# Performance work log

Measured on AMD Instinct MI355X. Metric: run time of the kernel, lower is better.

## Reference

```python
import jax, jax.numpy as jnp
import numpy as np

NUM_HEADS = 16
ROPE_BASE = 10000.0
NEG_INF = -1e9


def _layer_norm(x, g, b, eps=1e-5):
    mu = jnp.mean(x, axis=-1, keepdims=True)
    var = jnp.mean(jnp.square(x - mu), axis=-1, keepdims=True)
    return (x - mu) * jax.lax.rsqrt(var + eps) * g + b


def _rope_tables(seq_len, width):
    # theta_i = base^(-2i/width); tables shape (seq_len, width) with [m*theta, m*theta] concat
    theta = jnp.power(ROPE_BASE, -jnp.arange(0, width, 2, dtype=jnp.float32) / width)
    m_theta = jnp.arange(seq_len, dtype=jnp.float32)[:, None] * theta[None, :]
    m_theta = jnp.concatenate([m_theta, m_theta], axis=-1)
    return jnp.cos(m_theta), jnp.sin(m_theta)


def _apply_rope(x, cos, sin):
    # x: (BH, T, D); cos/sin: (T, D)
    half = x.shape[-1] // 2
    rot = jnp.concatenate([-x[..., half:], x[..., :half]], axis=-1)
    return cos[None] * x + sin[None] * rot


def setup_inputs() -> dict:
    key = jax.random.key(0)
    ks = jax.random.split(key, 6)
    T, B, C, F = 2048, 2, 1024, 4096
    s = 0.02
    return {
        "x": jax.random.normal(ks[0], (T, B, C), jnp.float32),
        "in_w": jax.random.normal(ks[1], (3 * C, C), jnp.float32) * s,
        "in_b": jnp.zeros((3 * C,), jnp.float32),
        "out_w": jax.random.normal(ks[2], (C, C), jnp.float32) * s,
        "out_b": jnp.zeros((C,), jnp.float32),
        "ln1_g": jnp.ones((C,), jnp.float32),
        "ln1_b": jnp.zeros((C,), jnp.float32),
        "ln2_g": jnp.ones((C,), jnp.float32),
        "ln2_b": jnp.zeros((C,), jnp.float32),
        "w1": jax.random.normal(ks[3], (F, C), jnp.float32) * s,
        "b1": jnp.zeros((F,), jnp.float32),
        "w2": jax.random.normal(ks[4], (C, F), jnp.float32) * s,
        "b2": jnp.zeros((C,), jnp.float32),
    }


def reference(x, in_w, in_b, out_w, out_b, ln1_g, ln1_b, ln2_g, ln2_b, w1, b1, w2, b2):
    # x: (T, B, C)  fairseq Time x Batch x Channel
    T, B, C = x.shape
    H = NUM_HEADS
    D = C // H

    # --- self-attention block (pre-LN) ---
    residual = x
    h = _layer_norm(x, ln1_g, ln1_b)
    qkv = h @ in_w.T + in_b                       # (T, B, 3C)
    q, k, v = jnp.split(qkv, 3, axis=-1)
    q = q * (D ** -0.5)

    def to_heads(t):  # (T, B, C) -> (B*H, T, D)
        return t.reshape(T, B * H, D).transpose(1, 0, 2)

    q, k, v = to_heads(q), to_heads(k), to_heads(v)
    cos, sin = _rope_tables(T, D)
    q = _apply_rope(q, cos, sin)
    k = _apply_rope(k, cos, sin)

    scores = jnp.einsum("btd,bsd->bts", q, k)     # (B*H, T, T)
    causal = jnp.triu(jnp.ones((T, T), dtype=bool), k=1)
    scores = jnp.where(causal[None], jnp.float32(NEG_INF), scores)
    attn = jax.nn.softmax(scores, axis=-1)
    o = jnp.einsum("bts,bsd->btd", attn, v)       # (B*H, T, D)
    o = o.transpose(1, 0, 2).reshape(T, B, C)
    o = o @ out_w.T + out_b
    x = residual + o

    # --- FFN block (pre-LN) ---
    residual = x
    h = _layer_norm(x, ln2_g, ln2_b)
    h = jax.nn.gelu(h @ w1.T + b1)
    h = h @ w2.T + b2
    return residual + h
```

## Files before the change

### kernel.cpp

```cpp
#include <hip/hip_runtime.h>
#include <hip/hip_bf16.h>
#include <math.h>

#define T_LEN 2048
#define B_SZ  2
#define C_DIM 1024
#define H_NUM 16
#define D_HEAD 64
#define F_DIM 4096
#define NT    (T_LEN * B_SZ)
#define BH    (B_SZ * H_NUM)
#define C3    (3 * C_DIM)

typedef __attribute__((ext_vector_type(8))) short short8v;
typedef __attribute__((ext_vector_type(4))) float f32x4;
typedef __hip_bfloat16 bf16;

__device__ __forceinline__ float bf2f(bf16 v) { return __bfloat162float(v); }
__device__ __forceinline__ bf16  f2bf(float f) { return __float2bfloat16(f); }
__device__ __forceinline__ short f2bfs(float f) { bf16 h = __float2bfloat16(f); return *(short*)&h; }
__device__ __forceinline__ void split2(float v, short& h, short& l) {
    bf16 hb = __float2bfloat16(v);
    bf16 lb = __float2bfloat16(v - __bfloat162float(hb));
    h = *(short*)&hb; l = *(short*)&lb;
}
__device__ __forceinline__ f32x4 mfma16(short8v a, short8v b, f32x4 c) {
    return __builtin_amdgcn_mfma_f32_16x16x32_bf16(a, b, c, 0, 0, 0);
}
__device__ __forceinline__ void async16(const void* g, void* lds) {
    __builtin_amdgcn_global_load_lds(
        (const __attribute__((address_space(1))) void*)g,
        (__attribute__((address_space(3))) void*)lds, 16, 0, 0);
}

__device__ __forceinline__ float block_sum_256(float val, float* sred) {
#pragma unroll
    for (int off = 32; off > 0; off >>= 1)
        val += __shfl_down(val, off, 64);
    int lane = threadIdx.x & 63;
    int wid  = threadIdx.x >> 6;
    if (lane == 0) sred[wid] = val;
    __syncthreads();
    float r = sred[0] + sred[1] + sred[2] + sred[3];
    __syncthreads();
    return r;
}

__global__ __launch_bounds__(256) void split_kernel(const float* __restrict__ src,
                                                    bf16* __restrict__ hi, bf16* __restrict__ lo) {
    int i = blockIdx.x * 256 + threadIdx.x;
    float4 v = ((const float4*)src)[i];
    short4 hv, lv;
    split2(v.x, hv.x, lv.x); split2(v.y, hv.y, lv.y);
    split2(v.z, hv.z, lv.z); split2(v.w, hv.w, lv.w);
    ((short4*)hi)[i] = hv;
    ((short4*)lo)[i] = lv;
}

__global__ __launch_bounds__(256) void ln_split_kernel(const float* __restrict__ x,
                                                       const float* __restrict__ g,
                                                       const float* __restrict__ b,
                                                       bf16* __restrict__ oh, bf16* __restrict__ ol) {
    __shared__ float sred[4];
    int row = blockIdx.x;
    int tid = threadIdx.x;
    const float* xr = x + (size_t)row * C_DIM;
    float4 xv = *(const float4*)(xr + tid * 4);
    float s = xv.x + xv.y + xv.z + xv.w;
    s = block_sum_256(s, sred);
    float mu = s * (1.0f / C_DIM);
    float d0 = xv.x - mu, d1 = xv.y - mu, d2 = xv.z - mu, d3 = xv.w - mu;
    float vs = d0 * d0 + d1 * d1 + d2 * d2 + d3 * d3;
    vs = block_sum_256(vs, sred);
    float rstd = rsqrtf(vs * (1.0f / C_DIM) + 1e-5f);
    float4 gv = *(const float4*)(g + tid * 4);
    float4 bv = *(const float4*)(b + tid * 4);
    float y0 = d0 * rstd * gv.x + bv.x, y1 = d1 * rstd * gv.y + bv.y;
    float y2 = d2 * rstd * gv.z + bv.z, y3 = d3 * rstd * gv.w + bv.w;
    short4 hv, lv;
    split2(y0, hv.x, lv.x); split2(y1, hv.y, lv.y);
    split2(y2, hv.z, lv.z); split2(y3, hv.w, lv.w);
    size_t base = (size_t)row * C_DIM / 4 + tid;
    ((short4*)oh)[base] = hv;
    ((short4*)ol)[base] = lv;
}

template <int EPI, bool ASPLIT, bool OUTBF16>
__global__ __launch_bounds__(256) void gemm_bf16(const bf16* __restrict__ Ah, const bf16* __restrict__ Al,
                                                 const bf16* __restrict__ Bh, const bf16* __restrict__ Bl,
                                                 const float* __restrict__ bias, const float* __restrict__ res,
                                                 float* __restrict__ Cf, bf16* __restrict__ Cb,
                                                 int N, int K) {
    constexpr int NBUF = ASPLIT ? 4 : 3;
    __shared__ __align__(16) char LDS[2][NBUF * 8192];

    int tid = threadIdx.x;
    int w = tid >> 6, l = tid & 63;
    int c = l & 15, g4 = l >> 4;
    int wm = w >> 1, wn = w & 1;
    int bn = blockIdx.x, bm = blockIdx.y;

    f32x4 acc[4][4];
#pragma unroll
    for (int i = 0; i < 4; i++)
#pragma unroll
        for (int j = 0; j < 4; j++) acc[i][j] = (f32x4){0.f, 0.f, 0.f, 0.f};

    const bf16* gB[4];
    gB[0] = Ah + (size_t)bm * 128 * K;
    gB[1] = Bh + (size_t)bn * 128 * K;
    gB[2] = Bl + (size_t)bn * 128 * K;
    gB[3] = ASPLIT ? (Al + (size_t)bm * 128 * K) : gB[0];
    const int NSEG = NBUF * 8;
    int lr4 = l >> 2, lc4 = l & 3;

    auto STAGE = [&](int kt, int pg) {
#pragma unroll
        for (int sidx = w; sidx < NSEG; sidx += 4) {
            int bsel = sidx >> 3, seg = sidx & 7;
            int r = seg * 16 + lr4;
            int cs = lc4 ^ ((r >> 1) & 3);
            const bf16* g = gB[bsel] + (size_t)r * K + kt + cs * 8;
            async16(g, LDS[pg] + bsel * 8192 + seg * 1024);
        }
    };

    STAGE(0, 0);
    __syncthreads();
    int cur = 0;
    for (int kt = 0; kt < K; kt += 32) {
        if (kt + 32 < K) STAGE(kt + 32, cur ^ 1);

        char* base = LDS[cur];
        char* LAhB = base;
        char* LBhB = base + 8192;
        char* LBlB = base + 16384;
        char* LAlB = base + 24576;

        short8v fah[4], fal[4], fbh[4], fbl[4];
#pragma unroll
        for (int i = 0; i < 4; i++) {
            int row = wm * 64 + i * 16 + c;
            int off = row * 64 + 16 * (g4 ^ ((row >> 1) & 3));
            fah[i] = *(const short8v*)(LAhB + off);
            if (ASPLIT) fal[i] = *(const short8v*)(LAlB + off);
        }
#pragma unroll
        for (int j = 0; j < 4; j++) {
            int row = wn * 64 + j * 16 + c;
            int off = row * 64 + 16 * (g4 ^ ((row >> 1) & 3));
            fbh[j] = *(const short8v*)(LBhB + off);
            fbl[j] = *(const short8v*)(LBlB + off);
        }
#pragma unroll
        for (int i = 0; i < 4; i++)
#pragma unroll
            for (int j = 0; j < 4; j++) {
                f32x4 t = acc[i][j];
                t = mfma16(fah[i], fbl[j], t);
                if (ASPLIT) t = mfma16(fal[i], fbh[j], t);
                t = mfma16(fah[i], fbh[j], t);
                acc[i][j] = t;
            }
        __syncthreads();
        cur ^= 1;
    }

#pragma unroll
    for (int i = 0; i < 4; i++)
#pragma unroll
        for (int j = 0; j < 4; j++) {
            int colg = bn * 128 + wn * 64 + j * 16 + c;
            float bv = bias[colg];
#pragma unroll
            for (int r = 0; r < 4; r++) {
                int rowg = bm * 128 + wm * 64 + i * 16 + g4 * 4 + r;
                float v = acc[i][j][r] + bv;
                if (EPI == 1) {
                    float t = tanhf(0.7978845608028654f * (v + 0.044715f * v * v * v));
                    v = 0.5f * v * (1.0f + t);
                } else if (EPI == 2) {
                    v += res[(size_t)rowg * N + colg];
                }
                if (OUTBF16) Cb[(size_t)rowg * N + colg] = f2bf(v);
                else         Cf[(size_t)rowg * N + colg] = v;
            }
        }
}

__global__ __launch_bounds__(256) void rope_kernel(const bf16* __restrict__ qkv,
                                                   bf16* __restrict__ Q, bf16* __restrict__ K) {
    int idx = blockIdx.x * 256 + threadIdx.x;
    int d  = idx & 31;
    int t  = (idx >> 5) & (T_LEN - 1);
    int bh = idx >> 16;
    int b  = bh >> 4;
    int h  = bh & 15;
    size_t row = (size_t)(t * B_SZ + b) * C3 + h * D_HEAD + d;
    float q0 = bf2f(qkv[row]),          q1 = bf2f(qkv[row + 32]);
    float k0 = bf2f(qkv[row + C_DIM]),  k1 = bf2f(qkv[row + C_DIM + 32]);
    q0 *= 0.125f; q1 *= 0.125f;
    float theta = exp2f((float)d * (-13.287712379549449f / 32.0f));
    float ang = (float)t * theta;
    float sn, cs;
    sincosf(ang, &sn, &cs);
    size_t ob = ((size_t)bh * T_LEN + t) * D_HEAD + d;
    Q[ob]      = f2bf(cs * q0 - sn * q1);
    Q[ob + 32] = f2bf(cs * q1 + sn * q0);
    K[ob]      = f2bf(cs * k0 - sn * k1);
    K[ob + 32] = f2bf(cs * k1 + sn * k0);
}

__global__ __launch_bounds__(256) void vt_kernel(const bf16* __restrict__ qkv, bf16* __restrict__ Vt) {
    __shared__ __align__(16) short L[64 * 64];
    char* LB = (char*)L;
    int qt = blockIdx.x, bh = blockIdx.y;
    int b = bh >> 4, h = bh & 15;
    int tid = threadIdx.x;
    int t0 = qt * 64;
#pragma unroll
    for (int e = 0; e < 2; e++) {
        int t = (tid >> 3) + e * 32, dc = tid & 7;
        short8v v = *(const short8v*)(qkv + (size_t)((t0 + t) * B_SZ + b) * C3 + 2 * C_DIM + h * 64 + dc * 8);
        *(short8v*)(LB + t * 128 + 16 * (dc ^ ((t >> 3) & 7))) = v;
    }
    __syncthreads();
    int d = tid & 63, tcb = tid >> 6;
    short8v v0, v1;
#pragma unroll
    for (int i = 0; i < 8; i++) {
        int t = tcb * 16 + i;
        v0[i] = *(const short*)(LB + t * 128 + 16 * ((d >> 3) ^ ((t >> 3) & 7)) + 2 * (d & 7));
    }
#pragma unroll
    for (int i = 0; i < 8; i++) {
        int t = tcb * 16 + 8 + i;
        v1[i] = *(const short*)(LB + t * 128 + 16 * ((d >> 3) ^ ((t >> 3) & 7)) + 2 * (d & 7));
    }
    bf16* op = Vt + ((size_t)bh * 64 + d) * T_LEN + t0 + tcb * 16;
    *(short8v*)(op)     = v0;
    *(short8v*)(op + 8) = v1;
}

__global__ __launch_bounds__(256) void attn_kernel(const bf16* __restrict__ Qg, const bf16* __restrict__ Kg,
                                                   const bf16* __restrict__ Vt,
                                                   bf16* __restrict__ Ohi, bf16* __restrict__ Olo) {
    __shared__ __align__(16) short Kl[64 * 64];
    __shared__ __align__(16) short Vl[64 * 64];
    __shared__ __align__(16) short Ps[4 * 16 * 64];
    char* KlB = (char*)Kl; char* VlB = (char*)Vl;
    int qt = gridDim.x - 1 - blockIdx.x;
    int bh = blockIdx.y;
    int tid = threadIdx.x;
    int w = tid >> 6, l = tid & 63;
    int c = l & 15, g4 = l >> 4;
    char* PsB = (char*)Ps + w * 2048;

    int q0 = qt * 64 + w * 16;
    const bf16* Qb = Qg + ((size_t)bh * T_LEN + q0 + c) * 64 + g4 * 8;
    short8v qf0 = *(const short8v*)(Qb);
    short8v qf1 = *(const short8v*)(Qb + 32);

    f32x4 oacc[4];
    float m_r[4], l_r[4];
#pragma unroll
    for (int i = 0; i < 4; i++) { oacc[i] = (f32x4){0.f,0.f,0.f,0.f}; m_r[i] = -1e30f; l_r[i] = 0.f; }

    int skv = tid >> 3, sc8 = tid & 7;
    for (int kt = 0; kt <= qt; kt++) {
        int kv0 = kt * 64;
        short8v kreg[2], vreg[2];
#pragma unroll
        for (int e = 0; e < 2; e++) {
            int rkv = skv + e * 32;
            kreg[e] = *(const short8v*)(Kg + ((size_t)bh * T_LEN + kv0 + rkv) * 64 + sc8 * 8);
            vreg[e] = *(const short8v*)(Vt + ((size_t)bh * 64 + rkv) * T_LEN + kv0 + sc8 * 8);
        }
        __syncthreads();
#pragma unroll
        for (int e = 0; e < 2; e++) {
            int rkv = skv + e * 32;
            *(short8v*)(KlB + rkv * 128 + 16 * (sc8 ^ (rkv & 7))) = kreg[e];
            *(short8v*)(VlB + rkv * 128 + 16 * (sc8 ^ (rkv & 7))) = vreg[e];
        }
        __syncthreads();

        f32x4 s[4];
#pragma unroll
        for (int j = 0; j < 4; j++) s[j] = (f32x4){0.f,0.f,0.f,0.f};
#pragma unroll
        for (int j = 0; j < 4; j++) {
            int row = j * 16 + c;
            short8v kb0 = *(const short8v*)(KlB + row * 128 + 16 * ((g4)     ^ (row & 7)));
            short8v kb1 = *(const short8v*)(KlB + row * 128 + 16 * ((4 + g4) ^ (row & 7)));
            s[j] = mfma16(qf0, kb0, s[j]);
            s[j] = mfma16(qf1, kb1, s[j]);
        }
        if (kt == qt) {
#pragma unroll
            for (int j = 0; j < 4; j++)
#pragma unroll
                for (int r = 0; r < 4; r++)
                    if (j * 16 + c > w * 16 + g4 * 4 + r) s[j][r] = -1e30f;
        }

#pragma unroll
        for (int r = 0; r < 4; r++) {
            float tm = fmaxf(fmaxf(s[0][r], s[1][r]), fmaxf(s[2][r], s[3][r]));
#pragma unroll
            for (int mk = 1; mk < 16; mk <<= 1) tm = fmaxf(tm, __shfl_xor(tm, mk, 64));
            float mnew = fmaxf(m_r[r], tm);
            float sc = __expf(m_r[r] - mnew);
            int q = g4 * 4 + r;
            float rs = 0.f;
#pragma unroll
            for (int j = 0; j < 4; j++) {
                float p = __expf(s[j][r] - mnew);
                rs += p;
                *(short*)(PsB + q * 128 + 16 * ((2 * j + (c >> 3)) ^ (q & 7)) + 2 * (c & 7)) = f2bfs(p);
            }
#pragma unroll
            for (int mk = 1; mk < 16; mk <<= 1) rs += __shfl_xor(rs, mk, 64);
            l_r[r] = l_r[r] * sc + rs;
            m_r[r] = mnew;
#pragma unroll
            for (int jd = 0; jd < 4; jd++) oacc[jd][r] *= sc;
        }
        __syncthreads();

#pragma unroll
        for (int ks = 0; ks < 2; ks++) {
            short8v pa = *(const short8v*)(PsB + c * 128 + 16 * ((ks * 4 + g4) ^ (c & 7)));
#pragma unroll
            for (int jd = 0; jd < 4; jd++) {
                int row = jd * 16 + c;
                short8v vb = *(const short8v*)(VlB + row * 128 + 16 * ((ks * 4 + g4) ^ (row & 7)));
                oacc[jd] = mfma16(pa, vb, oacc[jd]);
            }
        }
    }

    int b = bh >> 4, h = bh & 15;
#pragma unroll
    for (int r = 0; r < 4; r++) {
        float inv = 1.0f / l_r[r];
        int t = qt * 64 + w * 16 + g4 * 4 + r;
        size_t rb = (size_t)(t * B_SZ + b) * C_DIM + h * 64;
#pragma unroll
        for (int jd = 0; jd < 4; jd++) {
            float v = oacc[jd][r] * inv;
            short hs, ls;
            split2(v, hs, ls);
            *(short*)&Ohi[rb + jd * 16 + c] = hs;
            *(short*)&Olo[rb + jd * 16 + c] = ls;
        }
    }
}

extern "C" void kernel_launch(void* const* d_in, const int* in_sizes, int n_in,
                              void* d_out, int out_size, void* d_ws, size_t ws_size,
                              hipStream_t stream) {
    (void)in_sizes; (void)n_in; (void)out_size; (void)ws_size;
    const float* x     = (const float*)d_in[0];
    const float* in_w  = (const float*)d_in[1];
    const float* in_b  = (const float*)d_in[2];
    const float* out_w = (const float*)d_in[3];
    const float* out_b = (const float*)d_in[4];
    const float* ln1_g = (const float*)d_in[5];
    const float* ln1_b = (const float*)d_in[6];
    const float* ln2_g = (const float*)d_in[7];
    const float* ln2_b = (const float*)d_in[8];
    const float* w1    = (const float*)d_in[9];
    const float* b1    = (const float*)d_in[10];
    const float* w2    = (const float*)d_in[11];
    const float* b2    = (const float*)d_in[12];
    float* out = (float*)d_out;
    char* ws = (char*)d_ws;

    const size_t MB = 1 << 20;
    bf16* inw_h  = (bf16*)(ws + 0 * MB);
    bf16* inw_l  = (bf16*)(ws + 6 * MB);
    bf16* outw_h = (bf16*)(ws + 12 * MB);
    bf16* outw_l = (bf16*)(ws + 14 * MB);
    bf16* w1_h   = (bf16*)(ws + 16 * MB);
    bf16* w1_l   = (bf16*)(ws + 24 * MB);
    bf16* w2_h   = (bf16*)(ws + 32 * MB);
    bf16* w2_l   = (bf16*)(ws + 40 * MB);
    bf16* ln1o_h = (bf16*)(ws + 48 * MB);
    bf16* ln1o_l = (bf16*)(ws + 56 * MB);
    bf16* qkv    = (bf16*)(ws + 64 * MB);
    bf16* Qg     = (bf16*)(ws + 88 * MB);
    bf16* Kg     = (bf16*)(ws + 96 * MB);
    bf16* Vt     = (bf16*)(ws + 104 * MB);
    bf16* O_h    = (bf16*)(ws + 48 * MB);
    bf16* O_l    = (bf16*)(ws + 56 * MB);
    float* x2    = (float*)(ws + 112 * MB);
    bf16* h2_h   = (bf16*)(ws + 64 * MB);
    bf16* h2_l   = (bf16*)(ws + 72 * MB);
    bf16* f1     = (bf16*)(ws + 80 * MB);

    split_kernel<<<3072, 256, 0, stream>>>(in_w, inw_h, inw_l);
    split_kernel<<<1024, 256, 0, stream>>>(out_w, outw_h, outw_l);
    split_kernel<<<4096, 256, 0, stream>>>(w1, w1_h, w1_l);
    split_kernel<<<4096, 256, 0, stream>>>(w2, w2_h, w2_l);
    ln_split_kernel<<<NT, 256, 0, stream>>>(x, ln1_g, ln1_b, ln1o_h, ln1o_l);
    gemm_bf16<0, true, true><<<dim3(C3 / 128, NT / 128), 256, 0, stream>>>(
        ln1o_h, ln1o_l, inw_h, inw_l, in_b, nullptr, nullptr, qkv, C3, C_DIM);
    rope_kernel<<<(BH * T_LEN * 32) / 256, 256, 0, stream>>>(qkv, Qg, Kg);
    vt_kernel<<<dim3(T_LEN / 64, BH), 256, 0, stream>>>(qkv, Vt);
    attn_kernel<<<dim3(T_LEN / 64, BH), 256, 0, stream>>>(Qg, Kg, Vt, O_h, O_l);
    gemm_bf16<2, true, false><<<dim3(C_DIM / 128, NT / 128), 256, 0, stream>>>(
        O_h, O_l, outw_h, outw_l, out_b, x, x2, nullptr, C_DIM, C_DIM);
    ln_split_kernel<<<NT, 256, 0, stream>>>(x2, ln2_g, ln2_b, h2_h, h2_l);
    gemm_bf16<1, true, true><<<dim3(F_DIM / 128, NT / 128), 256, 0, stream>>>(
        h2_h, h2_l, w1_h, w1_l, b1, nullptr, nullptr, f1, F_DIM, C_DIM);
    gemm_bf16<2, false, false><<<dim3(C_DIM / 128, NT / 128), 256, 0, stream>>>(
        f1, nullptr, w2_h, w2_l, b2, x2, out, nullptr, C_DIM, F_DIM);
}
```

Measured before the change: 624.5 us.

## Pair causal query tiles per block and prefetch next K/V tile into registers

Each attention block now processes two query tiles (qt and NQT-1-qt) so every block does the same amount of causal work, halving the grid. The K/V loads for the next kv tile are issued into registers right after the current tile is stored to LDS, overlapping global latency with the QK/softmax/PV compute. This targets causal load imbalance and exposed memory latency in the attention loop, at the cost of fewer blocks in flight and extra live registers.

```diff
diff --git a/kernel.cpp b/kernel.cpp
--- a/kernel.cpp
+++ b/kernel.cpp
@@ -11,6 +11,7 @@
 #define NT    (T_LEN * B_SZ)
 #define BH    (B_SZ * H_NUM)
 #define C3    (3 * C_DIM)
+#define NQT   (T_LEN / 64)
 
 typedef __attribute__((ext_vector_type(8))) short short8v;
 typedef __attribute__((ext_vector_type(4))) float f32x4;
@@ -249,110 +250,127 @@
     __shared__ __align__(16) short Vl[64 * 64];
     __shared__ __align__(16) short Ps[4 * 16 * 64];
     char* KlB = (char*)Kl; char* VlB = (char*)Vl;
-    int qt = gridDim.x - 1 - blockIdx.x;
     int bh = blockIdx.y;
     int tid = threadIdx.x;
     int w = tid >> 6, l = tid & 63;
     int c = l & 15, g4 = l >> 4;
     char* PsB = (char*)Ps + w * 2048;
-
-    int q0 = qt * 64 + w * 16;
-    const bf16* Qb = Qg + ((size_t)bh * T_LEN + q0 + c) * 64 + g4 * 8;
-    short8v qf0 = *(const short8v*)(Qb);
-    short8v qf1 = *(const short8v*)(Qb + 32);
-
-    f32x4 oacc[4];
-    float m_r[4], l_r[4];
-#pragma unroll
-    for (int i = 0; i < 4; i++) { oacc[i] = (f32x4){0.f,0.f,0.f,0.f}; m_r[i] = -1e30f; l_r[i] = 0.f; }
-
     int skv = tid >> 3, sc8 = tid & 7;
-    for (int kt = 0; kt <= qt; kt++) {
-        int kv0 = kt * 64;
-        short8v kreg[2], vreg[2];
+    int b = bh >> 4, h = bh & 15;
+
+    const bf16* Kbase = Kg + (size_t)bh * T_LEN * 64;
+    const bf16* Vbase = Vt + (size_t)bh * 64 * T_LEN;
+
+#pragma unroll 1
+    for (int ph = 0; ph < 2; ph++) {
+        int qt = ph ? (NQT - 1 - blockIdx.x) : blockIdx.x;
+
+        int q0 = qt * 64 + w * 16;
+        const bf16* Qb = Qg + ((size_t)bh * T_LEN + q0 + c) * 64 + g4 * 8;
+        short8v qf0 = *(const short8v*)(Qb);
+        short8v qf1 = *(const short8v*)(Qb + 32);
+
+        f32x4 oacc[4];
+        float m_r[4], l_r[4];
+#pragma unroll
+        for (int i = 0; i < 4; i++) { oacc[i] = (f32x4){0.f,0.f,0.f,0.f}; m_r[i] = -1e30f; l_r[i] = 0.f; }
+
+        short8v kcur[2], vcur[2];
 #pragma unroll
         for (int e = 0; e < 2; e++) {
             int rkv = skv + e * 32;
-            kreg[e] = *(const short8v*)(Kg + ((size_t)bh * T_LEN + kv0 + rkv) * 64 + sc8 * 8);
-            vreg[e] = *(const short8v*)(Vt + ((size_t)bh * 64 + rkv) * T_LEN + kv0 + sc8 * 8);
-        }
-        __syncthreads();
-#pragma unroll
-        for (int e = 0; e < 2; e++) {
-            int rkv = skv + e * 32;
-            *(short8v*)(KlB + rkv * 128 + 16 * (sc8 ^ (rkv & 7))) = kreg[e];
-            *(short8v*)(VlB + rkv * 128 + 16 * (sc8 ^ (rkv & 7))) = vreg[e];
-        }
-        __syncthreads();
-
-        f32x4 s[4];
-#pragma unroll
-        for (int j = 0; j < 4; j++) s[j] = (f32x4){0.f,0.f,0.f,0.f};
-#pragma unroll
-        for (int j = 0; j < 4; j++) {
-            int row = j * 16 + c;
-            short8v kb0 = *(const short8v*)(KlB + row * 128 + 16 * ((g4)     ^ (row & 7)));
-            short8v kb1 = *(const short8v*)(KlB + row * 128 + 16 * ((4 + g4) ^ (row & 7)));
-            s[j] = mfma16(qf0, kb0, s[j]);
-            s[j] = mfma16(qf1, kb1, s[j]);
-        }
-        if (kt == qt) {
-#pragma unroll
-            for (int j = 0; j < 4; j++)
-#pragma unroll
-                for (int r = 0; r < 4; r++)
-                    if (j * 16 + c > w * 16 + g4 * 4 + r) s[j][r] = -1e30f;
+            kcur[e] = *(const short8v*)(Kbase + (size_t)rkv * 64 + sc8 * 8);
+            vcur[e] = *(const short8v*)(Vbase + (size_t)rkv * T_LEN + sc8 * 8);
+        }
+
+        for (int kt = 0; kt <= qt; kt++) {
+            __syncthreads();
+#pragma unroll
+            for (int e = 0; e < 2; e++) {
+                int rkv = skv + e * 32;
+                *(short8v*)(KlB + rkv * 128 + 16 * (sc8 ^ (rkv & 7))) = kcur[e];
+                *(short8v*)(VlB + rkv * 128 + 16 * (sc8 ^ (rkv & 7))) = vcur[e];
+            }
+            __syncthreads();
+
+            if (kt < qt) {
+                int kv1 = (kt + 1) * 64;
+#pragma unroll
+                for (int e = 0; e < 2; e++) {
+                    int rkv = skv + e * 32;
+                    kcur[e] = *(const short8v*)(Kbase + (size_t)(kv1 + rkv) * 64 + sc8 * 8);
+                    vcur[e] = *(const short8v*)(Vbase + (size_t)rkv * T_LEN + kv1 + sc8 * 8);
+                }
+            }
+
+            f32x4 s[4];
+#pragma unroll
+            for (int j = 0; j < 4; j++) s[j] = (f32x4){0.f,0.f,0.f,0.f};
+#pragma unroll
+            for (int j = 0; j < 4; j++) {
+                int row = j * 16 + c;
+                short8v kb0 = *(const short8v*)(KlB + row * 128 + 16 * ((g4)     ^ (row & 7)));
+                short8v kb1 = *(const short8v*)(KlB + row * 128 + 16 * ((4 + g4) ^ (row & 7)));
+                s[j] = mfma16(qf0, kb0, s[j]);
+                s[j] = mfma16(qf1, kb1, s[j]);
+            }
+            if (kt == qt) {
+#pragma unroll
+                for (int j = 0; j < 4; j++)
+#pragma unroll
+                    for (int r = 0; r < 4; r++)
+                        if (j * 16 + c > w * 16 + g4 * 4 + r) s[j][r] = -1e30f;
+            }
+
+#pragma unroll
+            for (int r = 0; r < 4; r++) {
+                float tm = fmaxf(fmaxf(s[0][r], s[1][r]), fmaxf(s[2][r], s[3][r]));
+#pragma unroll
+                for (int mk = 1; mk < 16; mk <<= 1) tm = fmaxf(tm, __shfl_xor(tm, mk, 64));
+                float mnew = fmaxf(m_r[r], tm);
+                float sc = __expf(m_r[r] - mnew);
+                int q = g4 * 4 + r;
+                float rs = 0.f;
+#pragma unroll
+                for (int j = 0; j < 4; j++) {
+                    float p = __expf(s[j][r] - mnew);
+                    rs += p;
+                    *(short*)(PsB + q * 128 + 16 * ((2 * j + (c >> 3)) ^ (q & 7)) + 2 * (c & 7)) = f2bfs(p);
+                }
+#pragma unroll
+                for (int mk = 1; mk < 16; mk <<= 1) rs += __shfl_xor(rs, mk, 64);
+                l_r[r] = l_r[r] * sc + rs;
+                m_r[r] = mnew;
+#pragma unroll
+                for (int jd = 0; jd < 4; jd++) oacc[jd][r] *= sc;
+            }
+            __syncthreads();
+
+#pragma unroll
+            for (int ks = 0; ks < 2; ks++) {
+                short8v pa = *(const short8v*)(PsB + c * 128 + 16 * ((ks * 4 + g4) ^ (c & 7)));
+#pragma unroll
+                for (int jd = 0; jd < 4; jd++) {
+                    int row = jd * 16 + c;
+                    short8v vb = *(const short8v*)(VlB + row * 128 + 16 * ((ks * 4 + g4) ^ (row & 7)));
+                    oacc[jd] = mfma16(pa, vb, oacc[jd]);
+                }
+            }
         }
 
 #pragma unroll
         for (int r = 0; r < 4; r++) {
-            float tm = fmaxf(fmaxf(s[0][r], s[1][r]), fmaxf(s[2][r], s[3][r]));
-#pragma unroll
-            for (int mk = 1; mk < 16; mk <<= 1) tm = fmaxf(tm, __shfl_xor(tm, mk, 64));
-            float mnew = fmaxf(m_r[r], tm);
-            float sc = __expf(m_r[r] - mnew);
-            int q = g4 * 4 + r;
-            float rs = 0.f;
-#pragma unroll
-            for (int j = 0; j < 4; j++) {
-                float p = __expf(s[j][r] - mnew);
-                rs += p;
-                *(short*)(PsB + q * 128 + 16 * ((2 * j + (c >> 3)) ^ (q & 7)) + 2 * (c & 7)) = f2bfs(p);
-            }
-#pragma unroll
-            for (int mk = 1; mk < 16; mk <<= 1) rs += __shfl_xor(rs, mk, 64);
-            l_r[r] = l_r[r] * sc + rs;
-            m_r[r] = mnew;
-#pragma unroll
-            for (int jd = 0; jd < 4; jd++) oacc[jd][r] *= sc;
-        }
-        __syncthreads();
-
-#pragma unroll
-        for (int ks = 0; ks < 2; ks++) {
-            short8v pa = *(const short8v*)(PsB + c * 128 + 16 * ((ks * 4 + g4) ^ (c & 7)));
+            float inv = 1.0f / l_r[r];
+            int t = qt * 64 + w * 16 + g4 * 4 + r;
+            size_t rb = (size_t)(t * B_SZ + b) * C_DIM + h * 64;
 #pragma unroll
             for (int jd = 0; jd < 4; jd++) {
-                int row = jd * 16 + c;
-                short8v vb = *(const short8v*)(VlB + row * 128 + 16 * ((ks * 4 + g4) ^ (row & 7)));
-                oacc[jd] = mfma16(pa, vb, oacc[jd]);
-            }
-        }
-    }
-
-    int b = bh >> 4, h = bh & 15;
-#pragma unroll
-    for (int r = 0; r < 4; r++) {
-        float inv = 1.0f / l_r[r];
-        int t = qt * 64 + w * 16 + g4 * 4 + r;
-        size_t rb = (size_t)(t * B_SZ + b) * C_DIM + h * 64;
-#pragma unroll
-        for (int jd = 0; jd < 4; jd++) {
-            float v = oacc[jd][r] * inv;
-            short hs, ls;
-            split2(v, hs, ls);
-            *(short*)&Ohi[rb + jd * 16 + c] = hs;
-            *(short*)&Olo[rb + jd * 16 + c] = ls;
+                float v = oacc[jd][r] * inv;
+                short hs, ls;
+                split2(v, hs, ls);
+                *(short*)&Ohi[rb + jd * 16 + c] = hs;
+                *(short*)&Olo[rb + jd * 16 + c] = ls;
+            }
         }
     }
 }
@@ -408,7 +426,7 @@
         ln1o_h, ln1o_l, inw_h, inw_l, in_b, nullptr, nullptr, qkv, C3, C_DIM);
     rope_kernel<<<(BH * T_LEN * 32) / 256, 256, 0, stream>>>(qkv, Qg, Kg);
     vt_kernel<<<dim3(T_LEN / 64, BH), 256, 0, stream>>>(qkv, Vt);
-    attn_kernel<<<dim3(T_LEN / 64, BH), 256, 0, stream>>>(Qg, Kg, Vt, O_h, O_l);
+    attn_kernel<<<dim3(NQT / 2, BH), 256, 0, stream>>>(Qg, Kg, Vt, O_h, O_l);
     gemm_bf16<2, true, false><<<dim3(C_DIM / 128, NT / 128), 256, 0, stream>>>(
         O_h, O_l, outw_h, outw_l, out_b, x, x2, nullptr, C_DIM, C_DIM);
     ln_split_kernel<<<NT, 256, 0, stream>>>(x2, ln2_g, ln2_b, h2_h, h2_l);
```

Result: faster. 548.2 us (-12.2%).
